# Performance work log

Measured on AMD Instinct MI355X. Metric: run time of the kernel, lower is better.

## Reference

```python
import jax, jax.numpy as jnp
import numpy as np

N = 20000   # nodes
E = 320000  # edges per relation
R = 4       # relations
H = 4       # attention heads
HID = 64    # hidden_dim1
DIN = 256   # input_dim
OUT = 64    # output_dim
NEG_SLOPE = 0.2  # PyG GATv2Conv default


def setup_inputs() -> dict:
    key = jax.random.key(0)
    ks = jax.random.split(key, 16)
    rn = lambda k, s: jax.random.normal(k, s, jnp.float32) * 0.05
    return {
        "x": jax.random.normal(ks[0], (N, DIN), jnp.float32),
        "edge_indices": jax.random.randint(ks[1], (R, 2, E), 0, N, jnp.int32),
        "Wl1": rn(ks[2], (R, DIN, H * HID)),
        "Wr1": rn(ks[3], (R, DIN, H * HID)),
        "att1": rn(ks[4], (R, H, HID)),
        "b1": rn(ks[5], (R, H * HID)),
        "Wl2": rn(ks[6], (R, H * HID, H * HID)),
        "Wr2": rn(ks[7], (R, H * HID, H * HID)),
        "att2": rn(ks[8], (R, H, HID)),
        "b2": rn(ks[9], (R, H * HID)),
        "Wrel3": rn(ks[10], (R, H * HID, HID)),
        "Wroot3": rn(ks[11], (R, H * HID, HID)),
        "b3": rn(ks[12], (R, HID)),
        "Wrel4": rn(ks[13], (R, HID, OUT)),
        "Wroot4": rn(ks[14], (R, HID, OUT)),
        "b4": rn(ks[15], (R, OUT)),
    }


def gatv2(x, src, dst, Wl, Wr, att, bias):
    """PyG GATv2Conv (concat heads, add_self_loops=True, share_weights=False)."""
    n = x.shape[0]
    loop = jnp.arange(n, dtype=src.dtype)
    src = jnp.concatenate([src, loop])  # add self loops
    dst = jnp.concatenate([dst, loop])
    xl = (x @ Wl).reshape(n, H, -1)  # source transform [N,H,C]
    xr = (x @ Wr).reshape(n, H, -1)  # target transform [N,H,C]
    z = jax.nn.leaky_relu(xl[src] + xr[dst], NEG_SLOPE)  # [E',H,C]
    e = jnp.einsum('ehc,hc->eh', z, att)                 # per-edge logits
    m = jax.ops.segment_max(e, dst, num_segments=n)
    m = jnp.where(jnp.isfinite(m), m, 0.0)
    p = jnp.exp(e - m[dst])
    s = jax.ops.segment_sum(p, dst, num_segments=n)
    alpha = p / s[dst]                                   # segment softmax
    out = jax.ops.segment_sum(alpha[:, :, None] * xl[src], dst, num_segments=n)
    return out.reshape(n, -1) + bias


def graphconv(x, src, dst, Wrel, Wroot, b):
    """PyG GraphConv: W1 x_i + W2 sum_j x_j (aggr='add')."""
    agg = jax.ops.segment_sum(x[src], dst, num_segments=x.shape[0])
    return agg @ Wrel + b + x @ Wroot


def reference(x, edge_indices, Wl1, Wr1, att1, b1, Wl2, Wr2, att2, b2,
              Wrel3, Wroot3, b3, Wrel4, Wroot4, b4):
    outs = []
    for i in range(R):  # small fixed relation count
        src, dst = edge_indices[i, 0], edge_indices[i, 1]
        h = jax.nn.relu(gatv2(x, src, dst, Wl1[i], Wr1[i], att1[i], b1[i]))
        h = jax.nn.relu(gatv2(h, src, dst, Wl2[i], Wr2[i], att2[i], b2[i]))
        h = jax.nn.relu(graphconv(h, src, dst, Wrel3[i], Wroot3[i], b3[i]))
        h = graphconv(h, src, dst, Wrel4[i], Wroot4[i], b4[i])
        outs.append(h[:, None, :])
    return jnp.concatenate(outs, axis=1)  # [N, R, OUT]
```

## Files before the change

kernel.cpp:

```cpp
#include <hip/hip_runtime.h>
#include <hip/hip_fp16.h>
#include <math.h>

#define NN   20000
#define EE   320000
#define RR   4

typedef unsigned short u16;
typedef unsigned int   u32;
typedef _Float16 half8v __attribute__((ext_vector_type(8)));
typedef _Float16 v2h    __attribute__((ext_vector_type(2)));
typedef __attribute__((ext_vector_type(4))) float f32x4;

static __device__ __forceinline__ u16 f2h(float f){ return __half_as_ushort(__float2half_rn(f)); }
static __device__ __forceinline__ v2h u2v(u32 u){ union{u32 u; v2h v;} c; c.u=u; return c.v; }
static __device__ __forceinline__ u32 v2u(v2h v){ union{u32 u; v2h v;} c; c.v=v; return c.u; }
static __device__ __forceinline__ v2h splat2(float f){ v2h r; r[0]=(_Float16)f; r[1]=(_Float16)f; return r; }
static __device__ __forceinline__ float fdot2(v2h a, v2h b, float c){
  return __builtin_amdgcn_fdot2(a, b, c, false);
}
static __device__ __forceinline__ void gload_lds16(const void* g, void* l){
  __builtin_amdgcn_global_load_lds((const __attribute__((address_space(1))) void*)g,
                                   (__attribute__((address_space(3))) void*)l, 16, 0, 0);
}

__global__ void k_zero_int(int* __restrict__ p, int n){
  int i = blockIdx.x*blockDim.x + threadIdx.x;
  if (i < n) p[i] = 0;
}
__global__ void k_countA(const int* __restrict__ ei, int* __restrict__ deg4){
  int i = blockIdx.x*blockDim.x + threadIdx.x;
  if (i < RR*EE) {
    int r = i / EE, e = i % EE;
    int d = ei[(size_t)r*2*EE + EE + e];
    atomicAdd(&deg4[r*NN + d], 1);
  }
}
__global__ __launch_bounds__(1024) void k_scan(const int* __restrict__ cnt_all, int* __restrict__ off_all,
                                               int* __restrict__ cur_all, int n){
  const int* cnt = cnt_all + (size_t)blockIdx.x*n;
  int* off = off_all + (size_t)blockIdx.x*(n+1);
  int* cur = cur_all + (size_t)blockIdx.x*n;
  __shared__ int part[1024];
  int t = threadIdx.x;
  int chunk = (n + 1023) >> 10;
  int lo = t*chunk; if (lo > n) lo = n;
  int hi = lo + chunk; if (hi > n) hi = n;
  int s = 0;
  for (int i = lo; i < hi; ++i) s += cnt[i];
  part[t] = s;
  __syncthreads();
  for (int d = 1; d < 1024; d <<= 1) {
    int u = (t >= d) ? part[t-d] : 0;
    __syncthreads();
    part[t] += u;
    __syncthreads();
  }
  int run = (t == 0) ? 0 : part[t-1];
  for (int i = lo; i < hi; ++i) { off[i] = run; cur[i] = run; run += cnt[i]; }
  if (t == 1023) off[n] = part[1023];
}
__global__ void k_scatterM(const int* __restrict__ ei, int* __restrict__ cur4, u32* __restrict__ csr4){
  int bid = blockIdx.x;
  int pass = bid / 5000;
  int i = (bid - pass*5000)*256 + threadIdx.x;
  int dlo = pass*5000, dhi = dlo + 5000;
  if (i < RR*EE) {
    int r = i / EE, e = i - r*EE;
    int d = ei[(size_t)r*2*EE + EE + e];
    if (d >= dlo && d < dhi) {
      int s = ei[(size_t)r*2*EE + e];
      int p = atomicAdd(&cur4[r*NN + d], 1);
      csr4[(size_t)r*EE + p] = (u32)s * 4096u;
    }
  }
}

static __device__ __forceinline__ void prep_body(const float* A, const float* B, u16* dst,
                                                 int K, int N, int total, int i){
  if (i >= total) return;
  int k = i % K;
  int n = (i / K) % (2*N);
  int r = i / (K*2*N);
  const float* S = (n < N) ? A : B;
  int nn = (n < N) ? n : n - N;
  dst[i] = f2h(S[((size_t)r*K + k)*N + nn]);
}
__global__ void k_prepall(const float* __restrict__ x, u16* __restrict__ xbf,
                          const float* __restrict__ Wl1, const float* __restrict__ Wr1, u16* __restrict__ W1T,
                          const float* __restrict__ Wl2, const float* __restrict__ Wr2, u16* __restrict__ W2T,
                          const float* __restrict__ W3a, const float* __restrict__ W3b, u16* __restrict__ W3T,
                          const float* __restrict__ W4a, const float* __restrict__ W4b, u16* __restrict__ W4T){
  int kind = blockIdx.y;
  int i = blockIdx.x*256 + threadIdx.x;
  if (kind == 0) {
    if (i < NN*256/4) {
      float4 v = reinterpret_cast<const float4*>(x)[i];
      ushort4 b;
      b.x = f2h(v.x); b.y = f2h(v.y); b.z = f2h(v.z); b.w = f2h(v.w);
      reinterpret_cast<ushort4*>(xbf)[i] = b;
    }
  } else if (kind == 1) prep_body(Wl1, Wr1, W1T, 256, 256, RR*512*256, i);
  else if (kind == 2)   prep_body(Wl2, Wr2, W2T, 256, 256, RR*512*256, i);
  else if (kind == 3)   prep_body(W3a, W3b, W3T, 256, 64,  RR*128*256, i);
  else                  prep_body(W4a, W4b, W4T, 64,  64,  RR*128*64,  i);
}

__global__ __launch_bounds__(256) void k_mfma(
    const u16* __restrict__ A, const u16* __restrict__ BT,
    int M, int K, u16* __restrict__ Cb, int ldc,
    long aZ, long btZ, long cZ)
{
  constexpr int BM = 128, BN = 128;
  constexpr int FI = 4, FJ = 4;
  const int zz = blockIdx.z;
  A  += (size_t)zz*aZ;
  BT += (size_t)zz*btZ;
  Cb += (size_t)zz*cZ;

  __shared__ u16 As[BM*32];
  __shared__ u16 Bs[BN*32];
  const int t = threadIdx.x;
  const int lane = t & 63, wid = t >> 6;
  const int wr = wid >> 1, wc = wid & 1;
  const int bm = blockIdx.x * BM, bn = blockIdx.y * BN;
  const int lr = lane & 15, lk = lane >> 4;

  f32x4 acc[FI][FJ];
  #pragma unroll
  for (int i = 0; i < FI; ++i)
    #pragma unroll
    for (int j = 0; j < FJ; ++j) acc[i][j] = (f32x4)(0.f);

  const int nk = K >> 5;
  char* AsB = (char*)As;
  char* BsB = (char*)Bs;

  for (int s = 0; s < nk; ++s) {
    const int kk = s << 5;
    #pragma unroll
    for (int i = 0; i < 2; ++i) {
      int c = t + 256*i;
      int row = c >> 2, sub = c & 3;
      int lsub = sub ^ (row & 3);
      int grow = bm + row; if (grow >= M) grow = M - 1;
      gload_lds16(A + (size_t)grow*K + kk + lsub*8, AsB + c*16);
    }
    #pragma unroll
    for (int i = 0; i < 2; ++i) {
      int c = t + 256*i;
      int row = c >> 2, sub = c & 3;
      int lsub = sub ^ (row & 3);
      gload_lds16(BT + (size_t)(bn + row)*K + kk + lsub*8, BsB + c*16);
    }
    __syncthreads();
    half8v a[FI], b[FJ];
    #pragma unroll
    for (int i = 0; i < FI; ++i) {
      int row = wr*64 + i*16 + lr;
      int sub = lk ^ (row & 3);
      a[i] = *reinterpret_cast<half8v*>(AsB + row*64 + sub*16);
    }
    #pragma unroll
    for (int j = 0; j < FJ; ++j) {
      int col = wc*64 + j*16 + lr;
      int sub = lk ^ (col & 3);
      b[j] = *reinterpret_cast<half8v*>(BsB + col*64 + sub*16);
    }
    #pragma unroll
    for (int i = 0; i < FI; ++i)
      #pragma unroll
      for (int j = 0; j < FJ; ++j)
        acc[i][j] = __builtin_amdgcn_mfma_f32_16x16x32_f16(a[i], b[j], acc[i][j], 0, 0, 0);
    __syncthreads();
  }

  #pragma unroll
  for (int i = 0; i < FI; ++i) {
    #pragma unroll
    for (int j = 0; j < FJ; ++j) {
      int col = bn + wc*64 + j*16 + lr;
      #pragma unroll
      for (int q = 0; q < 4; ++q) {
        int row = bm + wr*64 + i*16 + lk*4 + q;
        if (row < M) Cb[(size_t)row*ldc + col] = f2h(acc[i][j][q]);
      }
    }
  }
}

__global__ __launch_bounds__(256) void k_gat(
    const u16* __restrict__ xlr,
    const float* __restrict__ att, const float* __restrict__ bias,
    const int* __restrict__ off4, const u32* __restrict__ csr4,
    u16* __restrict__ out)
{
  const int bid = blockIdx.x;
  const int z = (bid & 7) >> 1;
  const int j4 = ((bid >> 3) << 1) | (bid & 1);
  const int node = j4*4 + (threadIdx.x >> 6);
  if (node >= NN) return;
  const int lane = threadIdx.x & 63;
  const int sl = lane & 31, sub = lane >> 5;
  const int* off = off4 + (size_t)z*(NN+1);
  const u32* csr = csr4 + (size_t)z*EE;
  u16* outp = out + (size_t)z*(size_t)NN*256;

  const int co = sl*8;
  const char* xc = (const char*)xlr + (size_t)z*1024 + co*2;
  const u16* selfrow = xlr + (size_t)z*512 + (size_t)node*2048;
  const v2h c02 = splat2(0.2f);
  const float L2E = 1.4426950408889634f;

  uint4 rx = *reinterpret_cast<const uint4*>(selfrow + 256 + co);
  v2h xr2[4] = {u2v(rx.x), u2v(rx.y), u2v(rx.z), u2v(rx.w)};
  v2h av2[4];
  {
    float4 q0 = *reinterpret_cast<const float4*>(att + z*256 + co);
    float4 q1 = *reinterpret_cast<const float4*>(att + z*256 + co + 4);
    av2[0][0]=(_Float16)(q0.x*L2E); av2[0][1]=(_Float16)(q0.y*L2E);
    av2[1][0]=(_Float16)(q0.z*L2E); av2[1][1]=(_Float16)(q0.w*L2E);
    av2[2][0]=(_Float16)(q1.x*L2E); av2[2][1]=(_Float16)(q1.y*L2E);
    av2[3][0]=(_Float16)(q1.z*L2E); av2[3][1]=(_Float16)(q1.w*L2E);
  }
  uint4 sx = *reinterpret_cast<const uint4*>(selfrow + co);
  v2h xs2[4] = {u2v(sx.x), u2v(sx.y), u2v(sx.z), u2v(sx.w)};
  float ps = 0.f;
  #pragma unroll
  for (int i = 0; i < 4; ++i) {
    v2h zz = xs2[i] + xr2[i];
    v2h lr = __builtin_elementwise_max(zz, zz*c02);
    ps = fdot2(av2[i], lr, ps);
  }
  ps += __shfl_xor(ps,1); ps += __shfl_xor(ps,2); ps += __shfl_xor(ps,4);
  float wsf = (sub == 0) ? exp2f(fminf(ps - 6.f, 12.f)) : 0.f;
  float s = wsf;
  v2h a2[4];
  {
    v2h w2 = splat2(wsf);
    #pragma unroll
    for (int i = 0; i < 4; ++i) a2[i] = w2*xs2[i];
  }

  const int e0 = off[node], e1 = off[node+1];
  const int kfull = e0 + ((e1 - e0) & ~7);
  for (int k = e0; k < kfull; k += 8) {
    v2h xv[4][4];
    float p[4];
    #pragma unroll
    for (int j = 0; j < 4; ++j) {
      u32 boff = csr[k + 2*j + sub];
      uint4 v = *reinterpret_cast<const uint4*>(xc + boff);
      xv[j][0]=u2v(v.x); xv[j][1]=u2v(v.y); xv[j][2]=u2v(v.z); xv[j][3]=u2v(v.w);
      float pp = 0.f;
      #pragma unroll
      for (int i = 0; i < 4; ++i) {
        v2h zz = xv[j][i] + xr2[i];
        v2h lr = __builtin_elementwise_max(zz, zz*c02);
        pp = fdot2(av2[i], lr, pp);
      }
      p[j] = pp;
    }
    #pragma unroll
    for (int j = 0; j < 4; ++j) {
      p[j] += __shfl_xor(p[j],1);
      p[j] += __shfl_xor(p[j],2);
      p[j] += __shfl_xor(p[j],4);
    }
    float w[4];
    #pragma unroll
    for (int j = 0; j < 4; ++j) w[j] = exp2f(fminf(p[j] - 6.f, 12.f));
    s += (w[0] + w[1]) + (w[2] + w[3]);
    #pragma unroll
    for (int j = 0; j < 4; ++j) {
      v2h w2 = splat2(w[j]);
      #pragma unroll
      for (int i = 0; i < 4; ++i) a2[i] += w2*xv[j][i];
    }
  }
  for (int k = kfull; k < e1; k += 2) {
    int kk = k + sub;
    bool val = kk < e1;
    u32 boff = csr[val ? kk : e1-1];
    uint4 v = *reinterpret_cast<const uint4*>(xc + boff);
    v2h xv[4] = {u2v(v.x), u2v(v.y), u2v(v.z), u2v(v.w)};
    float pp = 0.f;
    #pragma unroll
    for (int i = 0; i < 4; ++i) {
      v2h zz = xv[i] + xr2[i];
      v2h lr = __builtin_elementwise_max(zz, zz*c02);
      pp = fdot2(av2[i], lr, pp);
    }
    pp += __shfl_xor(pp,1); pp += __shfl_xor(pp,2); pp += __shfl_xor(pp,4);
    float w = val ? exp2f(fminf(pp - 6.f, 12.f)) : 0.f;
    s += w;
    v2h w2 = splat2(w);
    #pragma unroll
    for (int i = 0; i < 4; ++i) a2[i] += w2*xv[i];
  }
  s += __shfl_xor(s, 32);
  #pragma unroll
  for (int i = 0; i < 4; ++i) {
    u32 t = (u32)__shfl_xor((int)v2u(a2[i]), 32);
    a2[i] += u2v(t);
  }
  float inv = 1.f / s;
  if (sub == 0) {
    float4 b0 = *reinterpret_cast<const float4*>(bias + z*256 + co);
    float4 b1 = *reinterpret_cast<const float4*>(bias + z*256 + co + 4);
    float bv[8] = {b0.x,b0.y,b0.z,b0.w,b1.x,b1.y,b1.z,b1.w};
    u32 o[4];
    #pragma unroll
    for (int i = 0; i < 4; ++i) {
      float lo = fmaxf((float)a2[i][0]*inv + bv[2*i],   0.f);
      float hi = fmaxf((float)a2[i][1]*inv + bv[2*i+1], 0.f);
      o[i] = (u32)f2h(lo) | ((u32)f2h(hi) << 16);
    }
    uint4 ov = {o[0], o[1], o[2], o[3]};
    *reinterpret_cast<uint4*>(outp + (size_t)node*256 + co) = ov;
  }
}

template<int RELU, int F32OUT>
__global__ __launch_bounds__(256) void k_aggp(
    const u16* __restrict__ C, const float* __restrict__ bias,
    const int* __restrict__ off4, const u32* __restrict__ csr4,
    u16* __restrict__ outb, float* __restrict__ outf)
{
  const int bid = blockIdx.x;
  const int z = (bid & 7) >> 1;
  const int j4 = ((bid >> 3) << 1) | (bid & 1);
  const int node = j4*4 + (threadIdx.x >> 6);
  if (node >= NN) return;
  const int lane = threadIdx.x & 63;
  const int g = lane >> 4, sl = lane & 15;
  const u16* Cp = C + (size_t)z*(size_t)NN*128;
  const char* Cc = (const char*)Cp + sl*8;
  const int* off = off4 + (size_t)z*(NN+1);
  const u32* csr = csr4 + (size_t)z*EE;
  const int co = sl*4;
  v2h acc0 = splat2(0.f), acc1 = splat2(0.f);
  const int e0 = off[node], e1 = off[node+1];
  const int kfull = e0 + ((e1 - e0) & ~7);
  for (int k = e0; k < kfull; k += 8) {
    #pragma unroll
    for (int j = 0; j < 2; ++j) {
      u32 boff = csr[k + 2*g + j] >> 4;
      uint2 v = *reinterpret_cast<const uint2*>(Cc + boff);
      acc0 += u2v(v.x);
      acc1 += u2v(v.y);
    }
  }
  for (int k = kfull; k < e1; k += 4) {
    int kk = k + g;
    bool val = kk < e1;
    u32 boff = csr[val ? kk : e1-1] >> 4;
    uint2 v = *reinterpret_cast<const uint2*>(Cc + boff);
    acc0 += u2v(val ? v.x : 0u);
    acc1 += u2v(val ? v.y : 0u);
  }
  float a0 = (float)acc0[0], a1 = (float)acc0[1];
  float a2 = (float)acc1[0], a3 = (float)acc1[1];
  a0 += __shfl_xor(a0,16); a1 += __shfl_xor(a1,16);
  a2 += __shfl_xor(a2,16); a3 += __shfl_xor(a3,16);
  a0 += __shfl_xor(a0,32); a1 += __shfl_xor(a1,32);
  a2 += __shfl_xor(a2,32); a3 += __shfl_xor(a3,32);
  if (g == 0) {
    uint2 q = *reinterpret_cast<const uint2*>(Cp + (size_t)node*128 + 64 + co);
    v2h q0 = u2v(q.x), q1 = u2v(q.y);
    float4 bv = *reinterpret_cast<const float4*>(bias + z*64 + co);
    float v0 = a0 + (float)q0[0] + bv.x;
    float v1 = a1 + (float)q0[1] + bv.y;
    float v2 = a2 + (float)q1[0] + bv.z;
    float v3 = a3 + (float)q1[1] + bv.w;
    if (RELU) {
      v0 = fmaxf(v0, 0.f); v1 = fmaxf(v1, 0.f);
      v2 = fmaxf(v2, 0.f); v3 = fmaxf(v3, 0.f);
    }
    if (F32OUT) {
      float4 o = {v0, v1, v2, v3};
      *reinterpret_cast<float4*>(outf + (size_t)node*256 + z*64 + co) = o;
    } else {
      uint2 o;
      o.x = (u32)f2h(v0) | ((u32)f2h(v1) << 16);
      o.y = (u32)f2h(v2) | ((u32)f2h(v3) << 16);
      *reinterpret_cast<uint2*>(outb + ((size_t)z*NN + node)*64 + co) = o;
    }
  }
}

extern "C" void kernel_launch(void* const* d_in, const int* in_sizes, int n_in,
                              void* d_out, int out_size, void* d_ws, size_t ws_size,
                              hipStream_t stream)
{
  const float* x      = (const float*)d_in[0];
  const int*   ei     = (const int*)  d_in[1];
  const float* Wl1    = (const float*)d_in[2];
  const float* Wr1    = (const float*)d_in[3];
  const float* att1   = (const float*)d_in[4];
  const float* b1     = (const float*)d_in[5];
  const float* Wl2    = (const float*)d_in[6];
  const float* Wr2    = (const float*)d_in[7];
  const float* att2   = (const float*)d_in[8];
  const float* b2     = (const float*)d_in[9];
  const float* Wrel3  = (const float*)d_in[10];
  const float* Wroot3 = (const float*)d_in[11];
  const float* b3     = (const float*)d_in[12];
  const float* Wrel4  = (const float*)d_in[13];
  const float* Wroot4 = (const float*)d_in[14];
  const float* b4     = (const float*)d_in[15];
  float* out = (float*)d_out;

  const dim3 thr(256);
  const size_t NB2048 = (size_t)NN*2048;
  const size_t NB256  = (size_t)NN*256;
  const size_t NB128  = (size_t)NN*128;
  const size_t NB64   = (size_t)NN*64;

  u16* XLR = (u16*)d_ws;
  u16* h   = XLR + NB2048;
  u16* xbf = h   + NB256*RR;
  u16* W1T = xbf + NB256;
  u16* W2T = W1T + (size_t)RR*512*256;
  u16* W3T = W2T + (size_t)RR*512*256;
  u16* W4T = W3T + (size_t)RR*128*256;
  int* deg4 = (int*)(W4T + (size_t)RR*128*64);
  int* off4 = deg4 + RR*NN;
  int* cur4 = off4 + RR*(NN+1);
  u32* csr4 = (u32*)(cur4 + RR*NN);
  u16* C34 = XLR;
  u16* h3b = XLR + NB128*RR;

  k_prepall<<<dim3(5000,5), thr, 0, stream>>>(x, xbf, Wl1, Wr1, W1T, Wl2, Wr2, W2T,
                                              Wrel3, Wroot3, W3T, Wrel4, Wroot4, W4T);

  k_zero_int<<<dim3((RR*NN+255)/256), thr, 0, stream>>>(deg4, RR*NN);
  k_countA  <<<dim3((RR*EE+255)/256), thr, 0, stream>>>(ei, deg4);
  k_scan    <<<dim3(RR), dim3(1024), 0, stream>>>(deg4, off4, cur4, NN);
  k_scatterM<<<dim3(20000), thr, 0, stream>>>(ei, cur4, csr4);

  const dim3 gNode(20000);
  k_mfma<<<dim3(157,16,1), thr, 0, stream>>>(xbf, W1T, NN, 256, XLR, 2048, 0, 0, 0);
  k_gat<<<gNode, thr, 0, stream>>>(XLR, att1, b1, off4, csr4, h);
  k_mfma<<<dim3(157,4,RR), thr, 0, stream>>>(h, W2T, NN, 256, XLR, 2048,
                                             (long)NB256, 512*256, 512);
  k_gat<<<gNode, thr, 0, stream>>>(XLR, att2, b2, off4, csr4, h);
  k_mfma<<<dim3(157,1,RR), thr, 0, stream>>>(h, W3T, NN, 256, C34, 128,
                                             (long)NB256, 128*256, (long)NB128);
  k_aggp<1,0><<<gNode, thr, 0, stream>>>(C34, b3, off4, csr4, h3b, nullptr);
  k_mfma<<<dim3(157,1,RR), thr, 0, stream>>>(h3b, W4T, NN, 64, C34, 128,
                                             (long)NB64, 128*64, (long)NB128);
  k_aggp<0,1><<<gNode, thr, 0, stream>>>(C34, b4, off4, csr4, nullptr, out);
}
```

Measured before the change: 553.9 us.

## Split GAT work per head so each wave handles eight edges in parallel

The GAT kernel now assigns one wave per (relation, head, node) instead of one wave per (relation, node). Each 8-lane group covers the head's 64 channels and eight groups process eight edges at once, with cross-group reductions at the end. The grid grows fourfold, and the self/target row loads and output store switch to nontemporal. This trades more parallelism and shorter per-wave edge loops for four times as many CSR reads and a longer reduction tree.

```diff
diff --git a/kernel.cpp b/kernel.cpp
--- a/kernel.cpp
+++ b/kernel.cpp
@@ -10,6 +10,7 @@
 typedef unsigned int   u32;
 typedef _Float16 half8v __attribute__((ext_vector_type(8)));
 typedef _Float16 v2h    __attribute__((ext_vector_type(2)));
+typedef u32 u32x4 __attribute__((ext_vector_type(4)));
 typedef __attribute__((ext_vector_type(4))) float f32x4;
 
 static __device__ __forceinline__ u16 f2h(float f){ return __half_as_ushort(__float2half_rn(f)); }
@@ -196,35 +197,37 @@
     u16* __restrict__ out)
 {
   const int bid = blockIdx.x;
-  const int z = (bid & 7) >> 1;
-  const int j4 = ((bid >> 3) << 1) | (bid & 1);
-  const int node = j4*4 + (threadIdx.x >> 6);
-  if (node >= NN) return;
+  const bool h2 = bid >= 40000;
+  const int unit = (bid & 7) | (h2 ? 8 : 0);
+  const int z = unit >> 2, hh = unit & 3;
+  const int j = (h2 ? bid - 40000 : bid) >> 3;
+  const int node = j*4 + (threadIdx.x >> 6);
   const int lane = threadIdx.x & 63;
-  const int sl = lane & 31, sub = lane >> 5;
+  const int g = lane >> 3, gl = lane & 7;
+  const int co = gl*8;
+  const int colbase = z*512 + hh*64;
   const int* off = off4 + (size_t)z*(NN+1);
   const u32* csr = csr4 + (size_t)z*EE;
   u16* outp = out + (size_t)z*(size_t)NN*256;
 
-  const int co = sl*8;
-  const char* xc = (const char*)xlr + (size_t)z*1024 + co*2;
-  const u16* selfrow = xlr + (size_t)z*512 + (size_t)node*2048;
+  const char* xc = (const char*)xlr + (size_t)(colbase + co)*2;
+  const u16* selfrow = xlr + (size_t)node*2048 + colbase;
   const v2h c02 = splat2(0.2f);
   const float L2E = 1.4426950408889634f;
 
-  uint4 rx = *reinterpret_cast<const uint4*>(selfrow + 256 + co);
-  v2h xr2[4] = {u2v(rx.x), u2v(rx.y), u2v(rx.z), u2v(rx.w)};
   v2h av2[4];
   {
-    float4 q0 = *reinterpret_cast<const float4*>(att + z*256 + co);
-    float4 q1 = *reinterpret_cast<const float4*>(att + z*256 + co + 4);
+    float4 q0 = *reinterpret_cast<const float4*>(att + z*256 + hh*64 + co);
+    float4 q1 = *reinterpret_cast<const float4*>(att + z*256 + hh*64 + co + 4);
     av2[0][0]=(_Float16)(q0.x*L2E); av2[0][1]=(_Float16)(q0.y*L2E);
     av2[1][0]=(_Float16)(q0.z*L2E); av2[1][1]=(_Float16)(q0.w*L2E);
     av2[2][0]=(_Float16)(q1.x*L2E); av2[2][1]=(_Float16)(q1.y*L2E);
     av2[3][0]=(_Float16)(q1.z*L2E); av2[3][1]=(_Float16)(q1.w*L2E);
   }
-  uint4 sx = *reinterpret_cast<const uint4*>(selfrow + co);
-  v2h xs2[4] = {u2v(sx.x), u2v(sx.y), u2v(sx.z), u2v(sx.w)};
+  u32x4 rx = __builtin_nontemporal_load(reinterpret_cast<const u32x4*>(selfrow + 256 + co));
+  v2h xr2[4] = {u2v(rx[0]), u2v(rx[1]), u2v(rx[2]), u2v(rx[3])};
+  u32x4 sx = *reinterpret_cast<const u32x4*>(selfrow + co);
+  v2h xs2[4] = {u2v(sx[0]), u2v(sx[1]), u2v(sx[2]), u2v(sx[3])};
   float ps = 0.f;
   #pragma unroll
   for (int i = 0; i < 4; ++i) {
@@ -233,7 +236,7 @@
     ps = fdot2(av2[i], lr, ps);
   }
   ps += __shfl_xor(ps,1); ps += __shfl_xor(ps,2); ps += __shfl_xor(ps,4);
-  float wsf = (sub == 0) ? exp2f(fminf(ps - 6.f, 12.f)) : 0.f;
+  float wsf = (g == 0) ? exp2f(fminf(ps - 6.f, 12.f)) : 0.f;
   float s = wsf;
   v2h a2[4];
   {
@@ -243,47 +246,12 @@
   }
 
   const int e0 = off[node], e1 = off[node+1];
-  const int kfull = e0 + ((e1 - e0) & ~7);
-  for (int k = e0; k < kfull; k += 8) {
-    v2h xv[4][4];
-    float p[4];
-    #pragma unroll
-    for (int j = 0; j < 4; ++j) {
-      u32 boff = csr[k + 2*j + sub];
-      uint4 v = *reinterpret_cast<const uint4*>(xc + boff);
-      xv[j][0]=u2v(v.x); xv[j][1]=u2v(v.y); xv[j][2]=u2v(v.z); xv[j][3]=u2v(v.w);
-      float pp = 0.f;
-      #pragma unroll
-      for (int i = 0; i < 4; ++i) {
-        v2h zz = xv[j][i] + xr2[i];
-        v2h lr = __builtin_elementwise_max(zz, zz*c02);
-        pp = fdot2(av2[i], lr, pp);
-      }
-      p[j] = pp;
-    }
-    #pragma unroll
-    for (int j = 0; j < 4; ++j) {
-      p[j] += __shfl_xor(p[j],1);
-      p[j] += __shfl_xor(p[j],2);
-      p[j] += __shfl_xor(p[j],4);
-    }
-    float w[4];
-    #pragma unroll
-    for (int j = 0; j < 4; ++j) w[j] = exp2f(fminf(p[j] - 6.f, 12.f));
-    s += (w[0] + w[1]) + (w[2] + w[3]);
-    #pragma unroll
-    for (int j = 0; j < 4; ++j) {
-      v2h w2 = splat2(w[j]);
-      #pragma unroll
-      for (int i = 0; i < 4; ++i) a2[i] += w2*xv[j][i];
-    }
-  }
-  for (int k = kfull; k < e1; k += 2) {
-    int kk = k + sub;
+  for (int k = e0; k < e1; k += 8) {
+    int kk = k + g;
     bool val = kk < e1;
     u32 boff = csr[val ? kk : e1-1];
-    uint4 v = *reinterpret_cast<const uint4*>(xc + boff);
-    v2h xv[4] = {u2v(v.x), u2v(v.y), u2v(v.z), u2v(v.w)};
+    u32x4 v = *reinterpret_cast<const u32x4*>(xc + boff);
+    v2h xv[4] = {u2v(v[0]), u2v(v[1]), u2v(v[2]), u2v(v[3])};
     float pp = 0.f;
     #pragma unroll
     for (int i = 0; i < 4; ++i) {
@@ -298,26 +266,27 @@
     #pragma unroll
     for (int i = 0; i < 4; ++i) a2[i] += w2*xv[i];
   }
-  s += __shfl_xor(s, 32);
+  s += __shfl_xor(s,8); s += __shfl_xor(s,16); s += __shfl_xor(s,32);
   #pragma unroll
   for (int i = 0; i < 4; ++i) {
-    u32 t = (u32)__shfl_xor((int)v2u(a2[i]), 32);
-    a2[i] += u2v(t);
+    u32 t;
+    t = (u32)__shfl_xor((int)v2u(a2[i]), 8);  a2[i] += u2v(t);
+    t = (u32)__shfl_xor((int)v2u(a2[i]), 16); a2[i] += u2v(t);
+    t = (u32)__shfl_xor((int)v2u(a2[i]), 32); a2[i] += u2v(t);
   }
   float inv = 1.f / s;
-  if (sub == 0) {
-    float4 b0 = *reinterpret_cast<const float4*>(bias + z*256 + co);
-    float4 b1 = *reinterpret_cast<const float4*>(bias + z*256 + co + 4);
+  if (g == 0) {
+    float4 b0 = *reinterpret_cast<const float4*>(bias + z*256 + hh*64 + co);
+    float4 b1 = *reinterpret_cast<const float4*>(bias + z*256 + hh*64 + co + 4);
     float bv[8] = {b0.x,b0.y,b0.z,b0.w,b1.x,b1.y,b1.z,b1.w};
-    u32 o[4];
+    u32x4 ov;
     #pragma unroll
     for (int i = 0; i < 4; ++i) {
       float lo = fmaxf((float)a2[i][0]*inv + bv[2*i],   0.f);
       float hi = fmaxf((float)a2[i][1]*inv + bv[2*i+1], 0.f);
-      o[i] = (u32)f2h(lo) | ((u32)f2h(hi) << 16);
-    }
-    uint4 ov = {o[0], o[1], o[2], o[3]};
-    *reinterpret_cast<uint4*>(outp + (size_t)node*256 + co) = ov;
+      ov[i] = (u32)f2h(lo) | ((u32)f2h(hi) << 16);
+    }
+    __builtin_nontemporal_store(ov, reinterpret_cast<u32x4*>(outp + (size_t)node*256 + hh*64 + co));
   }
 }
 
@@ -439,16 +408,17 @@
   k_scan    <<<dim3(RR), dim3(1024), 0, stream>>>(deg4, off4, cur4, NN);
   k_scatterM<<<dim3(20000), thr, 0, stream>>>(ei, cur4, csr4);
 
-  const dim3 gNode(20000);
+  const dim3 gGat(80000);
+  const dim3 gAgg(20000);
   k_mfma<<<dim3(157,16,1), thr, 0, stream>>>(xbf, W1T, NN, 256, XLR, 2048, 0, 0, 0);
-  k_gat<<<gNode, thr, 0, stream>>>(XLR, att1, b1, off4, csr4, h);
+  k_gat<<<gGat, thr, 0, stream>>>(XLR, att1, b1, off4, csr4, h);
   k_mfma<<<dim3(157,4,RR), thr, 0, stream>>>(h, W2T, NN, 256, XLR, 2048,
                                              (long)NB256, 512*256, 512);
-  k_gat<<<gNode, thr, 0, stream>>>(XLR, att2, b2, off4, csr4, h);
+  k_gat<<<gGat, thr, 0, stream>>>(XLR, att2, b2, off4, csr4, h);
   k_mfma<<<dim3(157,1,RR), thr, 0, stream>>>(h, W3T, NN, 256, C34, 128,
                                              (long)NB256, 128*256, (long)NB128);
-  k_aggp<1,0><<<gNode, thr, 0, stream>>>(C34, b3, off4, csr4, h3b, nullptr);
+  k_aggp<1,0><<<gAgg, thr, 0, stream>>>(C34, b3, off4, csr4, h3b, nullptr);
   k_mfma<<<dim3(157,1,RR), thr, 0, stream>>>(h3b, W4T, NN, 64, C34, 128,
                                              (long)NB64, 128*64, (long)NB128);
-  k_aggp<0,1><<<gNode, thr, 0, stream>>>(C34, b4, off4, csr4, nullptr, out);
-}
+  k_aggp<0,1><<<gAgg, thr, 0, stream>>>(C34, b4, off4, csr4, nullptr, out);
+}
```

New measurement: 707.5 us. 27.7% more time.
